# Kernel tuning notes

Hardware: AMD Instinct MI355X
Metric: run time of the kernel (lower is better)

## Reference

```python
import jax, jax.numpy as jnp
import numpy as np

D = 20            # doc / proto-action feature dim (hard-coded via .view(slate_size, 20))
SLATE = 5
K = 100           # neighbors per slate element
N_DOCS = 1_000_000
HID = 256
SLOPE = 0.01      # F.leaky_relu default negative slope


def setup_inputs() -> dict:
    key = jax.random.key(0)
    ks = jax.random.split(key, 6)
    def lin_w(k, out_d, in_d):
        # kaiming-ish scale, matches torch Linear init magnitude roughly
        return jax.random.uniform(k, (out_d, in_d), jnp.float32, -1.0, 1.0) / np.sqrt(in_d)
    return {
        "input_state": jax.random.normal(ks[0], (D,), jnp.float32),
        "candidate_docs": jax.random.normal(ks[1], (N_DOCS, D), jnp.float32),
        "W1": lin_w(ks[2], HID, D),
        "b1": jnp.zeros((HID,), jnp.float32),
        "W2": lin_w(ks[3], HID, HID),
        "b2": jnp.zeros((HID,), jnp.float32),
        "W3": lin_w(ks[4], SLATE * D, HID),
        "b3": jnp.zeros((SLATE * D,), jnp.float32),
    }


def reference(input_state, candidate_docs, W1, b1, W2, b2, W3, b3):
    # --- actor policy net: Linear -> leaky_relu, x3 (leaky_relu also on output, as in source) ---
    x = input_state
    for W, b in ((W1, b1), (W2, b2), (W3, b3)):
        x = jax.nn.leaky_relu(x @ W.T + b, negative_slope=SLOPE)
    proto_slate = x.reshape(SLATE, D)                       # [slate, 20]

    # --- per-slate-element L2 distance to every candidate doc, vectorized ---
    # dists[s, n] = ||candidate_docs[n] - proto_slate[s]||_2
    diff = candidate_docs[None, :, :] - proto_slate[:, None, :]   # [slate, N, 20]
    dists = jnp.sqrt(jnp.sum(diff * diff, axis=-1))               # [slate, N]

    # top-k smallest distances (replaces full argsort + slice in the source)
    _, idx = jax.lax.top_k(-dists, K)                             # [slate, K]
    indices_tensor = idx.reshape(-1)                              # [slate*K], concat order as in source
    candidates_tensor = candidate_docs[indices_tensor]            # [slate*K, 20]
    return candidates_tensor, indices_tensor
```

## Files before the change

kernel.cpp:

```cpp
#include <hip/hip_runtime.h>
#include <stdint.h>
#include <math.h>

#define DDIM    20
#define SLATE   5
#define KSEL    100
#define HID     256
#define SAMPN   16384
#define NSH     8
#define SHCAP   1024
#define RCAP    8192
#define STP     128
#define OUT_IDX_OFF (SLATE * KSEL * DDIM)

#define WS_PROTO   0
#define WS_PROTOF  1024
#define WS_TP2     1536
#define WS_TM2     1556
#define WS_THI     1576
#define WS_SHCNT   1600
#define WS_STRICT  4160
#define WS_CNT2    6720
#define WS_ZEND    7040
#define WS_SKEYS   8192
#define WS_CAND    172032
#define WS_CAND2   335872
#define WS_STD2    499712
#define WS_STIX    540672
#define WS_STLEN   561152

__device__ __forceinline__ double dleaky(double x) { return x >= 0.0 ? x : 0.01 * x; }

__device__ __forceinline__ double calc_d2(const float* doc, const double* p) {
    double acc = 0.0;
#pragma unroll
    for (int i = 0; i < DDIM; ++i) {
        double d = (double)doc[i] - p[i];
        acc = fma(d, d, acc);
    }
    return acc;
}

__device__ __forceinline__ void load_doc(const float* __restrict__ docs,
                                         size_t n, float* doc) {
    const float4* dp = (const float4*)(docs + n * DDIM);
    float4 v0 = dp[0], v1 = dp[1], v2 = dp[2], v3 = dp[3], v4 = dp[4];
    doc[0] = v0.x; doc[1] = v0.y; doc[2] = v0.z; doc[3] = v0.w;
    doc[4] = v1.x; doc[5] = v1.y; doc[6] = v1.z; doc[7] = v1.w;
    doc[8] = v2.x; doc[9] = v2.y; doc[10] = v2.z; doc[11] = v2.w;
    doc[12] = v3.x; doc[13] = v3.y; doc[14] = v3.z; doc[15] = v3.w;
    doc[16] = v4.x; doc[17] = v4.y; doc[18] = v4.z; doc[19] = v4.w;
}

__device__ __forceinline__ int slate_use_primary(
    const unsigned* __restrict__ shardCnt, const unsigned* __restrict__ strictSh,
    int s) {
    unsigned strictTot = 0; bool ovf = false;
    for (int sh = 0; sh < NSH; ++sh) {
        if (shardCnt[(sh * SLATE + s) * 16] > SHCAP) ovf = true;
        strictTot += strictSh[(sh * SLATE + s) * 16];
    }
    return (strictTot >= KSEL) && !ovf;
}

__global__ __launch_bounds__(256) void mlp_sample_kernel(
    const float* __restrict__ x0, const float* __restrict__ docs,
    const float* __restrict__ W1, const float* __restrict__ b1,
    const float* __restrict__ W2, const float* __restrict__ b2,
    const float* __restrict__ W3, const float* __restrict__ b3,
    double* __restrict__ proto, float* __restrict__ protof,
    unsigned short* __restrict__ skeys, unsigned* __restrict__ zeroBase, int N) {
    const int bid = blockIdx.x, t = threadIdx.x;
    if (bid == SAMPN / 256) {
        for (int i = t; i < 1360; i += 256) zeroBase[i] = 0u;
        return;
    }
    __shared__ double xs[DDIM];
    __shared__ double h1[HID];
    __shared__ double h2[HID];
    __shared__ double ps[SLATE * DDIM];
    if (t < DDIM) xs[t] = (double)x0[t];
    __syncthreads();
    {
        double acc = 0.0;
#pragma unroll
        for (int i = 0; i < DDIM; ++i) acc = fma(xs[i], (double)W1[t * DDIM + i], acc);
        acc += (double)b1[t];
        h1[t] = dleaky(acc);
    }
    __syncthreads();
    {
        double acc = 0.0;
        for (int i = 0; i < HID; ++i) acc = fma(h1[i], (double)W2[t * HID + i], acc);
        acc += (double)b2[t];
        h2[t] = dleaky(acc);
    }
    __syncthreads();
    if (t < SLATE * DDIM) {
        double acc = 0.0;
        for (int i = 0; i < HID; ++i) acc = fma(h2[i], (double)W3[t * HID + i], acc);
        acc += (double)b3[t];
        double v = dleaky(acc);
        ps[t] = v;
        if (bid == 0) { proto[t] = v; protof[t] = (float)v; }
    }
    __syncthreads();
    int i = bid * 256 + t;
    if (i < SAMPN && i < N) {
        float doc[DDIM];
        load_doc(docs, (size_t)i, doc);
#pragma unroll
        for (int s = 0; s < SLATE; ++s) {
            double d2 = calc_d2(doc, ps + s * DDIM);
            skeys[s * SAMPN + i] = (unsigned short)(__float_as_uint((float)d2) >> 16);
        }
    }
}

__global__ __launch_bounds__(1024) void select_kernel(
    const unsigned short* __restrict__ skeys,
    unsigned short* __restrict__ Tp2, unsigned short* __restrict__ Tm2,
    unsigned short* __restrict__ Thi) {
    int s = blockIdx.x, t = threadIdx.x;
    int lane = t & 63, w = t >> 6;
    __shared__ unsigned wsum[2][16];
    const unsigned* kp = (const unsigned*)(skeys + (size_t)s * SAMPN);
    unsigned kw[8];
#pragma unroll
    for (int j = 0; j < 8; ++j) kw[j] = kp[j * 1024 + t];

    unsigned X10 = 0, X100 = 0;
    int buf = 0;
    for (int b = 15; b >= 0; --b) {
        unsigned p10 = X10 | (1u << b), p100 = X100 | (1u << b);
        int c10 = 0, c100 = 0;
#pragma unroll
        for (int j = 0; j < 8; ++j) {
            unsigned lo = kw[j] & 0xffffu, hi = kw[j] >> 16;
            c10  += (lo < p10)  + (hi < p10);
            c100 += (lo < p100) + (hi < p100);
        }
#pragma unroll
        for (int off = 32; off; off >>= 1) {
            c10  += __shfl_down(c10, off);
            c100 += __shfl_down(c100, off);
        }
        if (lane == 0) wsum[buf][w] = (unsigned)c10 | ((unsigned)c100 << 16);
        __syncthreads();
        unsigned t10 = 0, t100 = 0;
        for (int i = 0; i < 16; ++i) {
            unsigned v = wsum[buf][i];
            t10 += v & 0xffffu; t100 += v >> 16;
        }
        if ((int)t10 < 10)   X10 = p10;
        if ((int)t100 < 100) X100 = p100;
        buf ^= 1;
    }
    if (t == 0) {
        unsigned tp = X10 + 2u; if (tp > 65535u) tp = 65535u;
        Tp2[s] = (unsigned short)tp;
        Tm2[s] = (unsigned short)(X10 >= 2u ? X10 - 2u : 0u);
        Thi[s] = (unsigned short)X100;
    }
}

__global__ __launch_bounds__(256) void compact1_kernel(
    const float* __restrict__ docs, const float* __restrict__ protof,
    const unsigned short* __restrict__ Tp2, const unsigned short* __restrict__ Tm2,
    unsigned* __restrict__ shardCnt, unsigned* __restrict__ strictSh,
    unsigned* __restrict__ candIdx, int N) {
    __shared__ float psf[SLATE * DDIM];
    __shared__ unsigned short ktp[SLATE], ktm[SLATE];
    int t = threadIdx.x;
    if (t < SLATE * DDIM) psf[t] = protof[t];
    if (t < SLATE) { ktp[t] = Tp2[t]; ktm[t] = Tm2[t]; }
    __syncthreads();

    int n = blockIdx.x * 256 + t;
    bool dv = n < N;
    int lane = t & 63;
    int sh = blockIdx.x & (NSH - 1);

    float doc[DDIM];
    if (dv) load_doc(docs, (size_t)n, doc);
    else {
#pragma unroll
        for (int i = 0; i < DDIM; ++i) doc[i] = 0.f;
    }
    float acc[SLATE] = {0.f, 0.f, 0.f, 0.f, 0.f};
#pragma unroll
    for (int i = 0; i < DDIM; ++i) {
        float dvi = doc[i];
#pragma unroll
        for (int s = 0; s < SLATE; ++s) {
            float d = dvi - psf[s * DDIM + i];
            acc[s] = fmaf(d, d, acc[s]);
        }
    }
#pragma unroll
    for (int s = 0; s < SLATE; ++s) {
        unsigned k32 = __float_as_uint(acc[s]) >> 16;
        bool hit = dv && k32 <= (unsigned)ktp[s];
        unsigned long long ms = __ballot(dv && k32 <= (unsigned)ktm[s]);
        if (ms) {
            int ldr = __ffsll(ms) - 1;
            if (lane == ldr)
                atomicAdd(&strictSh[(sh * SLATE + s) * 16], (unsigned)__popcll(ms));
        }
        unsigned long long mh = __ballot(hit);
        if (mh) {
            int ldr = __ffsll(mh) - 1;
            unsigned base = 0;
            if (lane == ldr)
                base = atomicAdd(&shardCnt[(sh * SLATE + s) * 16], (unsigned)__popcll(mh));
            base = __shfl(base, ldr);
            if (hit) {
                unsigned pos = base + (unsigned)__popcll(mh & ((1ull << lane) - 1ull));
                if (pos < SHCAP)
                    candIdx[((size_t)(s * NSH + sh)) * SHCAP + pos] = (unsigned)n;
            }
        }
    }
}

__global__ __launch_bounds__(256) void rank_kernel(
    const float* __restrict__ docs, const double* __restrict__ proto,
    const unsigned short* __restrict__ Thi,
    const unsigned* __restrict__ shardCnt, const unsigned* __restrict__ strictSh,
    const unsigned* __restrict__ candIdx, unsigned* __restrict__ rscratch,
    double* __restrict__ stD2, unsigned* __restrict__ stIx,
    unsigned* __restrict__ stLen, int N) {
    const int sh = blockIdx.x, s = blockIdx.y, t = threadIdx.x;
    __shared__ double   ld[SHCAP];
    __shared__ unsigned li[SHCAP];
    __shared__ double   ps[DDIM];
    __shared__ double   outD2[KSEL];
    __shared__ unsigned outIx[KSEL];
    __shared__ unsigned c_s, rcnt;
    __shared__ int      prim_s;

    if (t < DDIM) ps[t] = proto[s * DDIM + t];
    if (t == 0) { prim_s = slate_use_primary(shardCnt, strictSh, s); rcnt = 0u; }
    __syncthreads();

    unsigned c;
    if (prim_s) {
        if (t == 0) {
            unsigned cc = shardCnt[(sh * SLATE + s) * 16];
            c_s = cc > SHCAP ? SHCAP : cc;
        }
        __syncthreads();
        c = c_s;
        const unsigned* src = candIdx + ((size_t)(s * NSH + sh)) * SHCAP;
        for (unsigned i = t; i < c; i += 256) {
            unsigned idx = src[i];
            li[i] = idx;
            float doc[DDIM];
            load_doc(docs, (size_t)idx, doc);
            ld[i] = calc_d2(doc, ps);
        }
    } else {
        unsigned kt = Thi[s];
        unsigned* lst = rscratch + (size_t)s * RCAP + (size_t)sh * SHCAP;
        int lo = (int)((long long)N * sh / NSH);
        int hi = (int)((long long)N * (sh + 1) / NSH);
        for (int n = lo + t; n < hi; n += 256) {
            float doc[DDIM];
            load_doc(docs, (size_t)n, doc);
            double d2 = calc_d2(doc, ps);
            unsigned key = __float_as_uint((float)d2) >> 16;
            if (key <= kt) {
                unsigned pos = atomicAdd(&rcnt, 1u);
                if (pos < SHCAP) lst[pos] = (unsigned)n;
            }
        }
        __syncthreads();
        c = rcnt < SHCAP ? rcnt : SHCAP;
        for (unsigned i = t; i < c; i += 256) {
            unsigned idx = lst[i];
            li[i] = idx;
            float doc[DDIM];
            load_doc(docs, (size_t)idx, doc);
            ld[i] = calc_d2(doc, ps);
        }
    }
    __syncthreads();

    for (unsigned e = t; e < c; e += 256) {
        double de = ld[e]; unsigned ie = li[e];
        unsigned rank = 0;
        unsigned j = 0;
        for (; j + 8 <= c; j += 8) {
            double d0 = ld[j+0], d1 = ld[j+1], d2 = ld[j+2], d3 = ld[j+3];
            double d4 = ld[j+4], d5 = ld[j+5], d6 = ld[j+6], d7 = ld[j+7];
            unsigned i0 = li[j+0], i1 = li[j+1], i2 = li[j+2], i3 = li[j+3];
            unsigned i4 = li[j+4], i5 = li[j+5], i6 = li[j+6], i7 = li[j+7];
            rank += ((d0 < de) || (d0 == de && i0 < ie))
                  + ((d1 < de) || (d1 == de && i1 < ie))
                  + ((d2 < de) || (d2 == de && i2 < ie))
                  + ((d3 < de) || (d3 == de && i3 < ie))
                  + ((d4 < de) || (d4 == de && i4 < ie))
                  + ((d5 < de) || (d5 == de && i5 < ie))
                  + ((d6 < de) || (d6 == de && i6 < ie))
                  + ((d7 < de) || (d7 == de && i7 < ie));
        }
        for (; j < c; ++j) {
            double dj = ld[j]; unsigned ij = li[j];
            rank += (dj < de) || (dj == de && ij < ie);
        }
        if (rank < KSEL) { outD2[rank] = de; outIx[rank] = ie; }
    }
    __syncthreads();

    unsigned L = c < KSEL ? c : KSEL;
    size_t base = (size_t)(s * NSH + sh) * STP;
    for (unsigned r = t; r < L; r += 256) {
        stD2[base + r] = outD2[r];
        stIx[base + r] = outIx[r];
    }
    if (t == 0) stLen[s * NSH + sh] = L;
}

__global__ __launch_bounds__(1024) void merge_kernel(
    const float* __restrict__ docs,
    const double* __restrict__ stD2, const unsigned* __restrict__ stIx,
    const unsigned* __restrict__ stLen, float* __restrict__ out) {
    int s = blockIdx.x, t = threadIdx.x;
    __shared__ double md[NSH * KSEL];
    __shared__ unsigned mi[NSH * KSEL];
    __shared__ unsigned Ls[NSH], offs[NSH + 1];
    __shared__ unsigned sel[KSEL];
    if (t < NSH) Ls[t] = stLen[s * NSH + t];
    __syncthreads();
    if (t == 0) {
        unsigned o = 0;
        for (int sh = 0; sh < NSH; ++sh) { offs[sh] = o; o += Ls[sh]; }
        offs[NSH] = o;
    }
    __syncthreads();
    for (int sh = 0; sh < NSH; ++sh) {
        unsigned L = Ls[sh];
        for (unsigned i = t; i < L; i += 1024) {
            md[sh * KSEL + i] = stD2[(size_t)(s * NSH + sh) * STP + i];
            mi[sh * KSEL + i] = stIx[(size_t)(s * NSH + sh) * STP + i];
        }
    }
    __syncthreads();

    unsigned S = offs[NSH];
    for (unsigned e = t; e < S; e += 1024) {
        int sh = 0;
        while (e >= offs[sh + 1]) ++sh;
        unsigned i = e - offs[sh];
        double xd = md[sh * KSEL + i];
        unsigned xi = mi[sh * KSEL + i];
        unsigned lo[NSH], hi[NSH];
#pragma unroll
        for (int so = 0; so < NSH; ++so) { lo[so] = 0; hi[so] = (so == sh) ? 0u : Ls[so]; }
        bool active = true;
        while (active) {
            active = false;
            double   dj[NSH];
            unsigned ij[NSH], mid[NSH];
#pragma unroll
            for (int so = 0; so < NSH; ++so) {
                if (lo[so] < hi[so]) {
                    unsigned m = (lo[so] + hi[so]) >> 1;
                    mid[so] = m;
                    dj[so] = md[so * KSEL + m];
                    ij[so] = mi[so * KSEL + m];
                }
            }
#pragma unroll
            for (int so = 0; so < NSH; ++so) {
                if (lo[so] < hi[so]) {
                    bool less = (dj[so] < xd) || (dj[so] == xd && ij[so] < xi);
                    if (less) lo[so] = mid[so] + 1; else hi[so] = mid[so];
                    if (lo[so] < hi[so]) active = true;
                }
            }
        }
        unsigned rank = i;
#pragma unroll
        for (int so = 0; so < NSH; ++so) rank += lo[so];
        if (rank < KSEL) sel[rank] = xi;
    }
    __syncthreads();

    if (t < KSEL) out[(size_t)OUT_IDX_OFF + s * KSEL + t] = (float)sel[t];
    for (int pos = t; pos < KSEL * DDIM; pos += 1024) {
        int r = pos / DDIM, c = pos % DDIM;
        out[((size_t)s * KSEL + r) * DDIM + c] = docs[(size_t)sel[r] * DDIM + c];
    }
}

extern "C" void kernel_launch(void* const* d_in, const int* in_sizes, int n_in,
                              void* d_out, int out_size, void* d_ws, size_t ws_size,
                              hipStream_t stream) {
    const float* x0   = (const float*)d_in[0];
    const float* docs = (const float*)d_in[1];
    const float* W1   = (const float*)d_in[2];
    const float* b1   = (const float*)d_in[3];
    const float* W2   = (const float*)d_in[4];
    const float* b2   = (const float*)d_in[5];
    const float* W3   = (const float*)d_in[6];
    const float* b3   = (const float*)d_in[7];
    int N = in_sizes[1] / DDIM;

    char* ws = (char*)d_ws;
    double*         proto    = (double*)(ws + WS_PROTO);
    float*          protof   = (float*)(ws + WS_PROTOF);
    unsigned short* Tp2      = (unsigned short*)(ws + WS_TP2);
    unsigned short* Tm2      = (unsigned short*)(ws + WS_TM2);
    unsigned short* Thi      = (unsigned short*)(ws + WS_THI);
    unsigned*       shardCnt = (unsigned*)(ws + WS_SHCNT);
    unsigned*       strictSh = (unsigned*)(ws + WS_STRICT);
    unsigned short* skeys    = (unsigned short*)(ws + WS_SKEYS);
    unsigned*       candIdx  = (unsigned*)(ws + WS_CAND);
    unsigned*       rscratch = (unsigned*)(ws + WS_CAND2);
    double*         stD2     = (double*)(ws + WS_STD2);
    unsigned*       stIx     = (unsigned*)(ws + WS_STIX);
    unsigned*       stLen    = (unsigned*)(ws + WS_STLEN);
    float*          outp     = (float*)d_out;

    mlp_sample_kernel<<<SAMPN / 256 + 1, 256, 0, stream>>>(
        x0, docs, W1, b1, W2, b2, W3, b3, proto, protof, skeys, shardCnt, N);
    select_kernel<<<SLATE, 1024, 0, stream>>>(skeys, Tp2, Tm2, Thi);
    int nb = (N + 255) / 256;
    compact1_kernel<<<nb, 256, 0, stream>>>(docs, protof, Tp2, Tm2,
                                            shardCnt, strictSh, candIdx, N);
    rank_kernel<<<dim3(NSH, SLATE), 256, 0, stream>>>(
        docs, proto, Thi, shardCnt, strictSh, candIdx, rscratch,
        stD2, stIx, stLen, N);
    merge_kernel<<<SLATE, 1024, 0, stream>>>(docs, stD2, stIx, stLen, outp);
}
```

Baseline: 92.38 us.

## Fuse MLP, sample-key computation and threshold selection into one head kernel

Merges the MLP+sampling kernel and the per-slate radix-select kernel into a single kernel with one 1024-thread block per slate element plus a zeroing block. Each block computes the MLP redundantly, computes 16 sample keys per thread for its own slate element in registers, and runs the bitwise threshold search directly, so the skeys round trip through global memory and one kernel launch go away. In exchange the MLP runs on only 6 blocks, and the 16384-doc sample pass is now spread over 5 CUs instead of 64 blocks, which could lengthen the head phase.

Result: slower. 101.1 us (+9.4%).

```diff
diff --git a/kernel.cpp b/kernel.cpp
--- a/kernel.cpp
+++ b/kernel.cpp
@@ -63,25 +63,28 @@
     return (strictTot >= KSEL) && !ovf;
 }
 
-__global__ __launch_bounds__(256) void mlp_sample_kernel(
+__global__ __launch_bounds__(1024) void head_kernel(
     const float* __restrict__ x0, const float* __restrict__ docs,
     const float* __restrict__ W1, const float* __restrict__ b1,
     const float* __restrict__ W2, const float* __restrict__ b2,
     const float* __restrict__ W3, const float* __restrict__ b3,
     double* __restrict__ proto, float* __restrict__ protof,
-    unsigned short* __restrict__ skeys, unsigned* __restrict__ zeroBase, int N) {
+    unsigned short* __restrict__ Tp2, unsigned short* __restrict__ Tm2,
+    unsigned short* __restrict__ Thi, unsigned* __restrict__ zeroBase, int N) {
     const int bid = blockIdx.x, t = threadIdx.x;
-    if (bid == SAMPN / 256) {
-        for (int i = t; i < 1360; i += 256) zeroBase[i] = 0u;
+    if (bid == SLATE) {
+        for (int i = t; i < 1360; i += 1024) zeroBase[i] = 0u;
         return;
     }
     __shared__ double xs[DDIM];
     __shared__ double h1[HID];
     __shared__ double h2[HID];
     __shared__ double ps[SLATE * DDIM];
+    __shared__ unsigned wsum[2][16];
+
     if (t < DDIM) xs[t] = (double)x0[t];
     __syncthreads();
-    {
+    if (t < HID) {
         double acc = 0.0;
 #pragma unroll
         for (int i = 0; i < DDIM; ++i) acc = fma(xs[i], (double)W1[t * DDIM + i], acc);
@@ -89,7 +92,7 @@
         h1[t] = dleaky(acc);
     }
     __syncthreads();
-    {
+    if (t < HID) {
         double acc = 0.0;
         for (int i = 0; i < HID; ++i) acc = fma(h1[i], (double)W2[t * HID + i], acc);
         acc += (double)b2[t];
@@ -105,40 +108,32 @@
         if (bid == 0) { proto[t] = v; protof[t] = (float)v; }
     }
     __syncthreads();
-    int i = bid * 256 + t;
-    if (i < SAMPN && i < N) {
-        float doc[DDIM];
-        load_doc(docs, (size_t)i, doc);
-#pragma unroll
-        for (int s = 0; s < SLATE; ++s) {
-            double d2 = calc_d2(doc, ps + s * DDIM);
-            skeys[s * SAMPN + i] = (unsigned short)(__float_as_uint((float)d2) >> 16);
-        }
-    }
-}
-
-__global__ __launch_bounds__(1024) void select_kernel(
-    const unsigned short* __restrict__ skeys,
-    unsigned short* __restrict__ Tp2, unsigned short* __restrict__ Tm2,
-    unsigned short* __restrict__ Thi) {
-    int s = blockIdx.x, t = threadIdx.x;
-    int lane = t & 63, w = t >> 6;
-    __shared__ unsigned wsum[2][16];
-    const unsigned* kp = (const unsigned*)(skeys + (size_t)s * SAMPN);
-    unsigned kw[8];
-#pragma unroll
-    for (int j = 0; j < 8; ++j) kw[j] = kp[j * 1024 + t];
-
+
+    const double* myp = ps + bid * DDIM;
+    unsigned short kk[16];
+#pragma unroll
+    for (int j = 0; j < 16; ++j) {
+        int idx = j * 1024 + t;
+        unsigned short key = 0xffffu;
+        if (idx < N) {
+            float doc[DDIM];
+            load_doc(docs, (size_t)idx, doc);
+            double d2 = calc_d2(doc, myp);
+            key = (unsigned short)(__float_as_uint((float)d2) >> 16);
+        }
+        kk[j] = key;
+    }
+
+    const int lane = t & 63, w = t >> 6;
     unsigned X10 = 0, X100 = 0;
     int buf = 0;
     for (int b = 15; b >= 0; --b) {
         unsigned p10 = X10 | (1u << b), p100 = X100 | (1u << b);
         int c10 = 0, c100 = 0;
 #pragma unroll
-        for (int j = 0; j < 8; ++j) {
-            unsigned lo = kw[j] & 0xffffu, hi = kw[j] >> 16;
-            c10  += (lo < p10)  + (hi < p10);
-            c100 += (lo < p100) + (hi < p100);
+        for (int j = 0; j < 16; ++j) {
+            c10  += ((unsigned)kk[j] < p10);
+            c100 += ((unsigned)kk[j] < p100);
         }
 #pragma unroll
         for (int off = 32; off; off >>= 1) {
@@ -158,9 +153,9 @@
     }
     if (t == 0) {
         unsigned tp = X10 + 2u; if (tp > 65535u) tp = 65535u;
-        Tp2[s] = (unsigned short)tp;
-        Tm2[s] = (unsigned short)(X10 >= 2u ? X10 - 2u : 0u);
-        Thi[s] = (unsigned short)X100;
+        Tp2[bid] = (unsigned short)tp;
+        Tm2[bid] = (unsigned short)(X10 >= 2u ? X10 - 2u : 0u);
+        Thi[bid] = (unsigned short)X100;
     }
 }
 
@@ -415,7 +410,6 @@
     unsigned short* Thi      = (unsigned short*)(ws + WS_THI);
     unsigned*       shardCnt = (unsigned*)(ws + WS_SHCNT);
     unsigned*       strictSh = (unsigned*)(ws + WS_STRICT);
-    unsigned short* skeys    = (unsigned short*)(ws + WS_SKEYS);
     unsigned*       candIdx  = (unsigned*)(ws + WS_CAND);
     unsigned*       rscratch = (unsigned*)(ws + WS_CAND2);
     double*         stD2     = (double*)(ws + WS_STD2);
@@ -423,9 +417,9 @@
     unsigned*       stLen    = (unsigned*)(ws + WS_STLEN);
     float*          outp     = (float*)d_out;
 
-    mlp_sample_kernel<<<SAMPN / 256 + 1, 256, 0, stream>>>(
-        x0, docs, W1, b1, W2, b2, W3, b3, proto, protof, skeys, shardCnt, N);
-    select_kernel<<<SLATE, 1024, 0, stream>>>(skeys, Tp2, Tm2, Thi);
+    head_kernel<<<SLATE + 1, 1024, 0, stream>>>(
+        x0, docs, W1, b1, W2, b2, W3, b3, proto, protof,
+        Tp2, Tm2, Thi, shardCnt, N);
     int nb = (N + 255) / 256;
     compact1_kernel<<<nb, 256, 0, stream>>>(docs, protof, Tp2, Tm2,
                                             shardCnt, strictSh, candIdx, N);
```
